# Performance work log

Measured on AMD Instinct MI355X. Metric: run time of the kernel, lower is better.

The kernel has to match this reference:

```python
import jax, jax.numpy as jnp
import numpy as np

SEQ_DIM = 256
PAIR_DIM = 128
HIDDEN = 32
B, L = 1, 384
EPS = 1e-5


def setup_inputs() -> dict:
    key = jax.random.key(0)
    ks = jax.random.split(key, 8)
    # xavier-normal-ish scales for the linear weights
    def xn(k, shape):
        fan_in, fan_out = shape[1], shape[0]
        std = (2.0 / (fan_in + fan_out)) ** 0.5
        return jax.random.normal(k, shape, dtype=jnp.float32) * std
    return {
        "seq": jax.random.normal(ks[0], (B, L, SEQ_DIM), dtype=jnp.float32),
        "ln_gamma": jnp.ones((SEQ_DIM,), dtype=jnp.float32),
        "ln_beta": jnp.zeros((SEQ_DIM,), dtype=jnp.float32),
        "w1": xn(ks[1], (HIDDEN, SEQ_DIM)),
        "b1": jnp.zeros((HIDDEN,), dtype=jnp.float32),
        "w2": xn(ks[2], (HIDDEN, SEQ_DIM)),
        "b2": jnp.zeros((HIDDEN,), dtype=jnp.float32),
        "w3": xn(ks[3], (PAIR_DIM, HIDDEN * HIDDEN)),
        "b3": jnp.zeros((PAIR_DIM,), dtype=jnp.float32),
    }


def reference(seq, ln_gamma, ln_beta, w1, b1, w2, b2, w3, b3):
    # LayerNorm over last dim (eps matches torch default 1e-5)
    mu = jnp.mean(seq, axis=-1, keepdims=True)
    var = jnp.mean(jnp.square(seq - mu), axis=-1, keepdims=True)
    x = (seq - mu) * jax.lax.rsqrt(var + EPS) * ln_gamma + ln_beta

    s1 = x @ w1.T + b1  # [B, L, H]
    s2 = x @ w2.T + b2  # [B, L, H]

    # pair[b,i,j,p] = sum_{d,f} s1[b,i,d] * s2[b,j,f] * w3[p, d*H+f] + b3[p]
    # Equivalent to einsum('bid,bjf->bijdf') -> view -> Linear, but contracted
    # directly without materializing the [B,L,L,H*H] intermediate.
    w3r = w3.reshape(PAIR_DIM, HIDDEN, HIDDEN)
    pair = jnp.einsum('bid,bjf,pdf->bijp', s1, s2, w3r) + b3
    return pair
```

## Files before the change

### kernel.cpp

```cpp
#include <hip/hip_runtime.h>
#include <hip/hip_bf16.h>


typedef __attribute__((ext_vector_type(8))) short short8;
typedef __attribute__((ext_vector_type(4))) short bf16x4;
typedef __attribute__((ext_vector_type(4))) float f32x4;

static __device__ __forceinline__ short f2bf(float f) {
    unsigned u = __float_as_uint(f);
    unsigned r = u + 0x7fffu + ((u >> 16) & 1u);
    return (short)(r >> 16);
}

__global__ __launch_bounds__(256) void ln_proj_cast_kernel(
    const float* __restrict__ seq, const float* __restrict__ gamma,
    const float* __restrict__ beta, const float* __restrict__ w1,
    const float* __restrict__ b1, const float* __restrict__ w2,
    const float* __restrict__ b2, const float* __restrict__ w3,
    short* __restrict__ s1, short* __restrict__ s2, short* __restrict__ w3c,
    int L) {
    const int t = threadIdx.x;

    if (blockIdx.x >= L) {
        int i = (blockIdx.x - L) * 256 + t;
        w3c[i] = f2bf(w3[i]);
        return;
    }

    const int row = blockIdx.x;
    const int wv = t >> 6;
    const int ln = t & 63;

    __shared__ float wsum[4];
    __shared__ float xln[256];
    __shared__ float part[4][64];

    float v = seq[row * 256 + t];

    float s = v;
    #pragma unroll
    for (int off = 32; off > 0; off >>= 1) s += __shfl_down(s, off);
    if (ln == 0) wsum[wv] = s;
    __syncthreads();
    float mean = (wsum[0] + wsum[1] + wsum[2] + wsum[3]) * (1.0f / 256.0f);

    float c = v - mean;
    float cs = c * c;
    #pragma unroll
    for (int off = 32; off > 0; off >>= 1) cs += __shfl_down(cs, off);
    __syncthreads();
    if (ln == 0) wsum[wv] = cs;
    __syncthreads();
    float var = (wsum[0] + wsum[1] + wsum[2] + wsum[3]) * (1.0f / 256.0f);

    float xn = c * rsqrtf(var + 1e-5f) * gamma[t] + beta[t];
    xln[t] = xn;
    __syncthreads();

    const float* w = (ln < 32) ? (w1 + ln * 256) : (w2 + (ln - 32) * 256);
    const f32x4* wp = (const f32x4*)(w + wv * 64);
    const float* xs = &xln[wv * 64];
    float p = 0.0f;
    #pragma unroll
    for (int i = 0; i < 16; ++i) {
        f32x4 w4 = wp[i];
        p += xs[4*i + 0] * w4.x + xs[4*i + 1] * w4.y +
             xs[4*i + 2] * w4.z + xs[4*i + 3] * w4.w;
    }
    part[wv][ln] = p;
    __syncthreads();

    if (t < 64) {
        float r = part[0][t] + part[1][t] + part[2][t] + part[3][t];
        if (t < 32) { r += b1[t];      s1[row * 32 + t]        = f2bf(r); }
        else        { r += b2[t - 32]; s2[row * 32 + (t - 32)] = f2bf(r); }
    }
}

template <typename OutT, bool BIAS, int MITERS>
__global__ __launch_bounds__(256, 4) void gemm_k32_kernel(
    const short* __restrict__ A, const short* __restrict__ B,
    OutT* __restrict__ D, const float* __restrict__ bias, int N) {
    const int lane = threadIdx.x & 63;
    const int wave = threadIdx.x >> 6;
    const int l15  = lane & 15;
    const int quad = lane >> 4;
    const int k0   = quad * 8;
    const int n0   = blockIdx.x * 64 + wave * 16;
    const int mbeg = blockIdx.y * (MITERS * 16);

    short8 bfrag = *reinterpret_cast<const short8*>(B + (size_t)(n0 + l15) * 32 + k0);

    f32x4 bv = {0.0f, 0.0f, 0.0f, 0.0f};
    if (BIAS) bv = *reinterpret_cast<const f32x4*>(bias + ((n0 + quad * 4) & 127));

    const short* aptr = A + (size_t)(mbeg + l15) * 32 + k0;
    OutT* dptr = D + (size_t)(mbeg + l15) * N + n0 + quad * 4;
    const size_t dstep = (size_t)16 * N;

    short8 a_cur = *reinterpret_cast<const short8*>(aptr);
    #pragma unroll
    for (int it = 0; it < MITERS; ++it) {
        aptr += 16 * 32;
        short8 a_nxt;
        if (it + 1 < MITERS) a_nxt = *reinterpret_cast<const short8*>(aptr);

        f32x4 acc = {0.0f, 0.0f, 0.0f, 0.0f};
        acc = __builtin_amdgcn_mfma_f32_16x16x32_bf16(bfrag, a_cur, acc, 0, 0, 0);

        if constexpr (BIAS) acc += bv;
        if constexpr (sizeof(OutT) == 4) {
            __builtin_nontemporal_store(acc, (f32x4*)dptr);
        } else {
            bf16x4 pv = { f2bf(acc.x), f2bf(acc.y), f2bf(acc.z), f2bf(acc.w) };
            *reinterpret_cast<bf16x4*>(dptr) = pv;
        }
        dptr += dstep;
        a_cur = a_nxt;
    }
}

extern "C" void kernel_launch(void* const* d_in, const int* in_sizes, int n_in,
                              void* d_out, int out_size, void* d_ws, size_t ws_size,
                              hipStream_t stream) {
    const float* seq   = (const float*)d_in[0];
    const float* gamma = (const float*)d_in[1];
    const float* beta  = (const float*)d_in[2];
    const float* w1    = (const float*)d_in[3];
    const float* b1    = (const float*)d_in[4];
    const float* w2    = (const float*)d_in[5];
    const float* b2    = (const float*)d_in[6];
    const float* w3    = (const float*)d_in[7];
    const float* b3    = (const float*)d_in[8];
    float* out = (float*)d_out;

    const int L = 384, H = 32, P = 128;
    const int N2 = P * H;
    const int N3 = L * P;

    char* ws = (char*)d_ws;
    short* s1  = (short*)(ws);
    short* s2  = (short*)(ws + 24576);
    short* w3c = (short*)(ws + 49152);
    short* T   = (short*)(ws + 311296);

    ln_proj_cast_kernel<<<L + (P * H * H) / 256, 256, 0, stream>>>(
        seq, gamma, beta, w1, b1, w2, b2, w3, s1, s2, w3c, L);

    gemm_k32_kernel<short, false, 3><<<dim3(N2 / 64, 8), 256, 0, stream>>>(
        s2, w3c, T, nullptr, N2);

    gemm_k32_kernel<float, true, 12><<<dim3(N3 / 64, 2), 256, 0, stream>>>(
        s1, T, out, b3, N3);
}
```

Before: 118.1 us.

## Fuse the two k32 GEMMs into one per-column pair kernel using LDS

Replaces the two-stage GEMM (s2 x w3 into a global bf16 intermediate T, then s1 x T with bias) with one kernel. Each block handles one output column j and half the rows. It first computes the 128x32 slice of T for that j with MFMA, stores it to LDS, then runs the s1 GEMM from LDS and writes the fp32 output with bias. This drops the global T round trip and one kernel launch. In exchange, each block recomputes T_j using mostly redundant MFMA lanes (only l15==0 results are kept), re-reads all of w3c from cache, and output stores are no longer nontemporal.

```diff
diff --git a/kernel.cpp b/kernel.cpp
--- a/kernel.cpp
+++ b/kernel.cpp
@@ -77,46 +77,59 @@
     }
 }
 
-template <typename OutT, bool BIAS, int MITERS>
-__global__ __launch_bounds__(256, 4) void gemm_k32_kernel(
-    const short* __restrict__ A, const short* __restrict__ B,
-    OutT* __restrict__ D, const float* __restrict__ bias, int N) {
-    const int lane = threadIdx.x & 63;
-    const int wave = threadIdx.x >> 6;
-    const int l15  = lane & 15;
-    const int quad = lane >> 4;
-    const int k0   = quad * 8;
-    const int n0   = blockIdx.x * 64 + wave * 16;
-    const int mbeg = blockIdx.y * (MITERS * 16);
+__global__ __launch_bounds__(256) void pair_fused_kernel(
+    const short* __restrict__ s1, const short* __restrict__ s2,
+    const short* __restrict__ w3c, const float* __restrict__ b3,
+    float* __restrict__ out) {
+    const int bx = blockIdx.x;
+    const int j = bx >> 1;
+    const int split = bx & 1;
+    const int t = threadIdx.x;
+    const int wv = t >> 6;
+    const int ln = t & 63;
+    const int l15 = ln & 15;
+    const int quad = ln >> 4;
+    const int k0 = quad * 8;
 
-    short8 bfrag = *reinterpret_cast<const short8*>(B + (size_t)(n0 + l15) * 32 + k0);
+    __shared__ short Tlds[128 * 40];
 
-    f32x4 bv = {0.0f, 0.0f, 0.0f, 0.0f};
-    if (BIAS) bv = *reinterpret_cast<const f32x4*>(bias + ((n0 + quad * 4) & 127));
+    short8 s2frag = *(const short8*)(s2 + j * 32 + k0);
+    #pragma unroll 4
+    for (int i = 0; i < 64; ++i) {
+        int n0 = (wv * 64 + i) * 16;
+        short8 wfrag = *(const short8*)(w3c + (size_t)(n0 + l15) * 32 + k0);
+        f32x4 acc = {0.0f, 0.0f, 0.0f, 0.0f};
+        acc = __builtin_amdgcn_mfma_f32_16x16x32_bf16(wfrag, s2frag, acc, 0, 0, 0);
+        if (l15 == 0) {
+            int base = n0 + quad * 4;
+            int p = base >> 5, d = base & 31;
+            bf16x4 pv = { f2bf(acc.x), f2bf(acc.y), f2bf(acc.z), f2bf(acc.w) };
+            *(bf16x4*)(&Tlds[p * 40 + d]) = pv;
+        }
+    }
+    __syncthreads();
 
-    const short* aptr = A + (size_t)(mbeg + l15) * 32 + k0;
-    OutT* dptr = D + (size_t)(mbeg + l15) * N + n0 + quad * 4;
-    const size_t dstep = (size_t)16 * N;
+    const int pw = wv;
+    short8 bf0 = *(const short8*)(&Tlds[(pw * 32 + l15) * 40 + k0]);
+    short8 bf1 = *(const short8*)(&Tlds[(pw * 32 + 16 + l15) * 40 + k0]);
+    f32x4 bv0 = *(const f32x4*)(b3 + pw * 32 + quad * 4);
+    f32x4 bv1 = *(const f32x4*)(b3 + pw * 32 + 16 + quad * 4);
 
-    short8 a_cur = *reinterpret_cast<const short8*>(aptr);
-    #pragma unroll
-    for (int it = 0; it < MITERS; ++it) {
-        aptr += 16 * 32;
-        short8 a_nxt;
-        if (it + 1 < MITERS) a_nxt = *reinterpret_cast<const short8*>(aptr);
+    const size_t N = 49152;
+    float* dbase = out + (size_t)(split * 192 + l15) * N + j * 128 + pw * 32 + quad * 4;
 
-        f32x4 acc = {0.0f, 0.0f, 0.0f, 0.0f};
-        acc = __builtin_amdgcn_mfma_f32_16x16x32_bf16(bfrag, a_cur, acc, 0, 0, 0);
+    #pragma unroll 3
+    for (int mt = 0; mt < 12; ++mt) {
+        int m0 = split * 192 + mt * 16;
+        short8 af = *(const short8*)(s1 + (size_t)(m0 + l15) * 32 + k0);
+        f32x4 acc0 = {0.0f, 0.0f, 0.0f, 0.0f};
+        f32x4 acc1 = {0.0f, 0.0f, 0.0f, 0.0f};
+        acc0 = __builtin_amdgcn_mfma_f32_16x16x32_bf16(bf0, af, acc0, 0, 0, 0);
+        acc1 = __builtin_amdgcn_mfma_f32_16x16x32_bf16(bf1, af, acc1, 0, 0, 0);
 
-        if constexpr (BIAS) acc += bv;
-        if constexpr (sizeof(OutT) == 4) {
-            __builtin_nontemporal_store(acc, (f32x4*)dptr);
-        } else {
-            bf16x4 pv = { f2bf(acc.x), f2bf(acc.y), f2bf(acc.z), f2bf(acc.w) };
-            *reinterpret_cast<bf16x4*>(dptr) = pv;
-        }
-        dptr += dstep;
-        a_cur = a_nxt;
+        float* dp = dbase + (size_t)mt * 16 * N;
+        *(f32x4*)dp        = acc0 + bv0;
+        *(f32x4*)(dp + 16) = acc1 + bv1;
     }
 }
 
@@ -135,21 +148,14 @@
     float* out = (float*)d_out;
 
     const int L = 384, H = 32, P = 128;
-    const int N2 = P * H;
-    const int N3 = L * P;
 
     char* ws = (char*)d_ws;
     short* s1  = (short*)(ws);
     short* s2  = (short*)(ws + 24576);
     short* w3c = (short*)(ws + 49152);
-    short* T   = (short*)(ws + 311296);
 
     ln_proj_cast_kernel<<<L + (P * H * H) / 256, 256, 0, stream>>>(
         seq, gamma, beta, w1, b1, w2, b2, w3, s1, s2, w3c, L);
 
-    gemm_k32_kernel<short, false, 3><<<dim3(N2 / 64, 8), 256, 0, stream>>>(
-        s2, w3c, T, nullptr, N2);
-
-    gemm_k32_kernel<float, true, 12><<<dim3(N3 / 64, 2), 256, 0, stream>>>(
-        s1, T, out, b3, N3);
+    pair_fused_kernel<<<L * 2, 256, 0, stream>>>(s1, s2, w3c, b3, out);
 }
```

Result: slower. 127.8 us (+8.3%).
